# Performance work log

Measured on AMD Instinct MI355X. Metric: run time of the kernel, lower is better.

## Reference

```python
import jax, jax.numpy as jnp
import numpy as np

WL_W = 8  # weight bit-width (wl_weight)
WL_A = 8  # activation bit-width (wl_activate)


def _wage_q(x, bits):
    """WAGE quantizer with straight-through estimator.

    Rounds to a grid of step 1/2^(bits-1) and clips to (-1+delta, 1-delta),
    matching NeuroSim's wage_quantizer Q/C composition and the detach-based
    STE used in QConv2d/QLinear's training (inference=0) path.
    """
    s = 2.0 ** (bits - 1)
    delta = 1.0 / s
    q = jnp.clip(jnp.round(x * s) / s, -1.0 + delta, 1.0 - delta)
    return x + jax.lax.stop_gradient(q - x)


def _qconv(x, w):
    # quantize weights -> 3x3 conv (stride 1, pad 1) -> quantize activations
    wq = _wage_q(w, WL_W)
    y = jax.lax.conv_general_dilated(
        x, wq, window_strides=(1, 1), padding=((1, 1), (1, 1)),
        dimension_numbers=('NCHW', 'OIHW', 'NCHW'))
    return _wage_q(y, WL_A)


def setup_inputs() -> dict:
    key = jax.random.key(0)
    ks = jax.random.split(key, 9)
    x = jax.random.normal(ks[0], (16, 4, 256, 256), dtype=jnp.float32)
    w1 = jax.random.normal(ks[1], (32, 4, 3, 3), dtype=jnp.float32) * 0.2
    ws = {f"w{i}": jax.random.normal(ks[i], (32, 32, 3, 3), dtype=jnp.float32) * 0.1
          for i in range(2, 8)}
    wfc = jax.random.normal(ks[8], (1, 32), dtype=jnp.float32) * 0.2
    return {"x": x, "w1": w1, **ws, "wfc": wfc}


def reference(x, w1, w2, w3, w4, w5, w6, w7, wfc):
    # 7 stacked quantized 3x3 convs, channels 4->32->...->32
    for w in (w1, w2, w3, w4, w5, w6, w7):
        x = _qconv(x, w)                    # [B,32,256,256]
    x = jnp.max(x, axis=(2, 3))             # MaxPool2d(256,256) == global max -> [B,32]
    wq = _wage_q(wfc, WL_W)
    y = x @ wq.T                             # QLinear 32 -> 1, [B,1]
    return _wage_q(y, WL_A)
```

## Files before the change

### kernel.cpp

```cpp
#include <hip/hip_runtime.h>

#define BB 16
#define HH 256
#define WW 256
#define PC 258
#define PP ((size_t)(PC * PC))

typedef int i32x4 __attribute__((ext_vector_type(4)));
typedef int i32x16 __attribute__((ext_vector_type(16)));
typedef float f32x16 __attribute__((ext_vector_type(16)));
typedef _Float16 f16x8 __attribute__((ext_vector_type(8)));

__global__ __launch_bounds__(256) void prep_kernel(
    const float* __restrict__ x, const float* __restrict__ w1,
    const float* __restrict__ w2, const float* __restrict__ w3,
    const float* __restrict__ w4, const float* __restrict__ w5,
    const float* __restrict__ w6, const float* __restrict__ w7,
    const float* __restrict__ wfc,
    _Float16* __restrict__ pre, _Float16* __restrict__ frag1,
    signed char* __restrict__ wfr, int* __restrict__ wfcq,
    int* __restrict__ gmax, signed char* __restrict__ A0) {
  int bid = blockIdx.x, tid = threadIdx.x;
  if (bid < 4096) {
    int px = bid * 256 + tid;
    int b = px >> 16, rem = px & 65535;
    int y = rem >> 8, xc = rem & 255;
    const float* xp = x + (size_t)b * 4 * 65536 + rem;
    f16x8 o;
#pragma unroll
    for (int ic = 0; ic < 4; ++ic) {
      float v = xp[ic * 65536];
      _Float16 hf = (_Float16)v;
      float r = v - (float)hf;
      o[ic * 2] = hf;
      o[ic * 2 + 1] = (_Float16)r;
    }
    *(f16x8*)(pre + ((size_t)b * PP + (size_t)(y + 1) * PC + (xc + 1)) * 8) = o;
  } else if (bid < 4312) {
    int i = (bid - 4096) * 256 + tid;
    int layer = i / 9216, within = i - layer * 9216;
    const float* w = layer == 0 ? w2 : layer == 1 ? w3 : layer == 2 ? w4
                   : layer == 3 ? w5 : layer == 4 ? w6 : w7;
    int t = within >> 10;
    int l = (within >> 4) & 63;
    int j = within & 15;
    int ic = (l >> 5) * 16 + j;
    int oc = l & 31;
    int q = (int)rintf(w[oc * 288 + ic * 9 + t] * 128.0f);
    q = min(127, max(-127, q));
    wfr[(size_t)layer * 9216 + within] = (signed char)q;
  } else if (bid == 4312) {
    for (int p = tid; p < 384; p += 256) {
      int s = p >> 6, l = p & 63;
      int dr = s >> 1, pp = s & 1;
      int oc = l & 31, half = l >> 5;
      int dx = pp * 2 + half;
#pragma unroll
      for (int j = 0; j < 8; ++j) {
        int ic = j >> 1;
        _Float16 v = (_Float16)0.f;
        if (!(pp == 1 && half == 1)) {
          int q = (int)rintf(w1[oc * 36 + ic * 9 + dr * 3 + dx] * 128.0f);
          q = min(127, max(-127, q));
          v = (_Float16)((float)q * 0.0078125f);
        }
        frag1[s * 512 + l * 8 + j] = v;
      }
    }
    if (tid < 32) {
      int q = (int)rintf(wfc[tid] * 128.0f);
      q = min(127, max(-127, q));
      wfcq[tid] = q;
    }
    for (int i2 = tid; i2 < 512; i2 += 256) gmax[i2] = -128;
  } else {
    int idx = (bid - 4313) * 256 + tid;
    if (idx < 16448) {
      int img = idx / 1028, p = idx - img * 1028;
      int row, col;
      if (p < 258) { row = 0; col = p; }
      else if (p < 516) { row = 257; col = p - 258; }
      else { int q2 = p - 516; row = 1 + (q2 & 255); col = (q2 >> 8) ? 257 : 0; }
      size_t off = (size_t)img * PP + (size_t)row * PC + col;
      f16x8 z16 = {};
      *(f16x8*)(pre + off * 8) = z16;
      i32x4 z = {};
      ((i32x4*)(A0 + off * 32))[0] = z;
      ((i32x4*)(A0 + off * 32 + 16))[0] = z;
    }
  }
}

__global__ __launch_bounds__(256) void pad_kernel(signed char* __restrict__ A1) {
  int idx = blockIdx.x * 256 + threadIdx.x;
  if (idx < 16448) {
    int img = idx / 1028, p = idx - img * 1028;
    int row, col;
    if (p < 258) { row = 0; col = p; }
    else if (p < 516) { row = 257; col = p - 258; }
    else { int q2 = p - 516; row = 1 + (q2 & 255); col = (q2 >> 8) ? 257 : 0; }
    size_t off = (size_t)img * PP + (size_t)row * PC + col;
    i32x4 z = {};
    ((i32x4*)(A1 + off * 32))[0] = z;
    ((i32x4*)(A1 + off * 32 + 16))[0] = z;
  }
}

__device__ __forceinline__ int pack4(int q0, int q1, int q2, int q3) {
  return (q0 & 255) | ((q1 & 255) << 8) | ((q2 & 255) << 16) | ((q3 & 255) << 24);
}

__device__ __forceinline__ int quant1(int a) {
  int q = (a + 63 + ((a >> 7) & 1)) >> 7;
  return min(127, max(-127, q));
}

__device__ __forceinline__ int quant_max(const i32x16& acc, int mymax) {
#pragma unroll
  for (int r = 0; r < 16; ++r) mymax = max(mymax, quant1(acc[r]));
  return mymax;
}

__device__ __forceinline__ i32x4 half_swap(int v0, int v1, int v2, int v3, int hi) {
  int s0 = hi ? v0 : v2;
  int s1 = hi ? v1 : v3;
  int r0 = __shfl_xor(s0, 32);
  int r1 = __shfl_xor(s1, 32);
  i32x4 ch;
  ch.x = hi ? r0 : v0;
  ch.y = hi ? v2 : r0;
  ch.z = hi ? r1 : v1;
  ch.w = hi ? v3 : r1;
  return ch;
}

__global__ __launch_bounds__(256) void conv1_mfma_kernel(
    const _Float16* __restrict__ pre, const _Float16* __restrict__ frag1,
    signed char* __restrict__ out) {
  int tid = threadIdx.x;
  int wi = tid >> 6;
  int l = tid & 63;
  int lo = l & 31;
  int hi = l >> 5;
  int b = blockIdx.z;
  int h0 = blockIdx.y * 2;
  int wbase = blockIdx.x * 128 + wi * 32;
  int w = wbase + lo;

  const f16x8* fp = (const f16x8*)frag1;
  f16x8 bf[6];
#pragma unroll
  for (int s = 0; s < 6; ++s) bf[s] = fp[s * 64 + l];

  f32x16 acc0 = {}, acc1 = {};

#pragma unroll
  for (int r = 0; r < 4; ++r) {
    const _Float16* rp = pre + ((size_t)b * PP + (size_t)(h0 + r) * PC) * 8;
#pragma unroll
    for (int p = 0; p < 2; ++p) {
      int col = w + p * 2 + hi;
      f16x8 av = {};
      if (!(p == 1 && hi == 1))
        av = *(const f16x8*)(rp + (size_t)col * 8);
      if (r < 3) acc0 = __builtin_amdgcn_mfma_f32_32x32x16_f16(bf[r * 2 + p], av, acc0, 0, 0, 0);
      if (r > 0) acc1 = __builtin_amdgcn_mfma_f32_32x32x16_f16(bf[(r - 1) * 2 + p], av, acc1, 0, 0, 0);
    }
  }

#pragma unroll
  for (int rr = 0; rr < 2; ++rr) {
    const f32x16& acc = rr ? acc1 : acc0;
    int q[16];
#pragma unroll
    for (int r = 0; r < 16; ++r) {
      int t = (int)rintf(acc[r] * 128.0f);
      q[r] = min(127, max(-127, t));
    }
    int v0 = pack4(q[0], q[1], q[2], q[3]);
    int v1 = pack4(q[4], q[5], q[6], q[7]);
    int v2 = pack4(q[8], q[9], q[10], q[11]);
    int v3 = pack4(q[12], q[13], q[14], q[15]);
    i32x4 ch = half_swap(v0, v1, v2, v3, hi);
    *(i32x4*)(out + ((size_t)b * PP + (size_t)(h0 + rr + 1) * PC + (w + 1)) * 32 + hi * 16) = ch;
  }
}

template <int MODE>
__global__ __launch_bounds__(512, 4) void conv_fused_kernel(
    const signed char* __restrict__ in, const signed char* __restrict__ fragA,
    const signed char* __restrict__ fragB, signed char* __restrict__ out,
    int* __restrict__ gmax) {
  __shared__ int Lint[6 * 2 * PC * 4];
  __shared__ int red[8][32];

  int tid = threadIdx.x;
  int wi = tid >> 6;
  int l = tid & 63;
  int lo = l & 31;
  int hi = l >> 5;
  int b = blockIdx.y;
  int hs = blockIdx.x * 4;
  int w = wi * 32 + lo;

  if (tid < 24) {
    int rr = tid >> 2, half = (tid >> 1) & 1, cs = tid & 1;
    i32x4 z = {};
    *(i32x4*)&Lint[((rr * 2 + half) * PC + (cs ? 257 : 0)) * 4] = z;
  }

  const i32x4* fpA = (const i32x4*)fragA;
  i32x4 bw[9];
#pragma unroll
  for (int t = 0; t < 9; ++t) bw[t] = fpA[t * 64 + l];

  int lanep = (w << 5) + (hi << 4);

  auto rowptr = [&](int yy) -> const signed char* {
    int prow = min(max(yy + 1, 0), 257);
    return in + ((size_t)b * PP + (size_t)prow * PC) * 32 + lanep;
  };

  auto lds_store_row = [&](const i32x16& acc, int rrel, bool valid) {
    int v0 = pack4(quant1(acc[0]), quant1(acc[1]), quant1(acc[2]), quant1(acc[3]));
    int v1 = pack4(quant1(acc[4]), quant1(acc[5]), quant1(acc[6]), quant1(acc[7]));
    int v2 = pack4(quant1(acc[8]), quant1(acc[9]), quant1(acc[10]), quant1(acc[11]));
    int v3 = pack4(quant1(acc[12]), quant1(acc[13]), quant1(acc[14]), quant1(acc[15]));
    i32x4 ch = half_swap(v0, v1, v2, v3, hi);
    if (!valid) ch = i32x4{};
    *(i32x4*)&Lint[((rrel * 2 + hi) * PC + (w + 1)) * 4] = ch;
  };

#pragma unroll 1
  for (int p = 0; p < 3; ++p) {
    int ar0 = hs - 1 + 2 * p;
    const signed char* rp[4];
#pragma unroll
    for (int rr = 0; rr < 4; ++rr) rp[rr] = rowptr(ar0 - 1 + rr);
    i32x4 rin[4][3];
#pragma unroll
    for (int rr = 0; rr < 4; ++rr)
#pragma unroll
      for (int dx = 0; dx < 3; ++dx)
        rin[rr][dx] = *(const i32x4*)(rp[rr] + dx * 32);

    i32x16 acc0 = {}, acc1 = {};
#pragma unroll
    for (int t = 0; t < 9; ++t) {
      int dy = t / 3, dx = t % 3;
      acc0 = __builtin_amdgcn_mfma_i32_32x32x32_i8(bw[t], rin[dy][dx], acc0, 0, 0, 0);
      acc1 = __builtin_amdgcn_mfma_i32_32x32x32_i8(bw[t], rin[dy + 1][dx], acc1, 0, 0, 0);
    }
    lds_store_row(acc0, 2 * p, (unsigned)ar0 < 256u);
    lds_store_row(acc1, 2 * p + 1, (unsigned)(ar0 + 1) < 256u);
  }

  const i32x4* fpB = (const i32x4*)fragB;
#pragma unroll
  for (int t = 0; t < 9; ++t) bw[t] = fpB[t * 64 + l];
  __syncthreads();

  int mymax = -128;
#pragma unroll 1
  for (int p = 0; p < 2; ++p) {
    i32x4 tp[4][3];
#pragma unroll
    for (int rr = 0; rr < 4; ++rr) {
      int rrel = 2 * p + rr;
#pragma unroll
      for (int dx = 0; dx < 3; ++dx)
        tp[rr][dx] = *(const i32x4*)&Lint[((rrel * 2 + hi) * PC + (w + dx)) * 4];
    }
    i32x16 acc0 = {}, acc1 = {};
#pragma unroll
    for (int t = 0; t < 9; ++t) {
      int dy = t / 3, dx = t % 3;
      if (MODE == 1) {
        acc0 = __builtin_amdgcn_mfma_i32_32x32x32_i8(tp[dy][dx], bw[t], acc0, 0, 0, 0);
        acc1 = __builtin_amdgcn_mfma_i32_32x32x32_i8(tp[dy + 1][dx], bw[t], acc1, 0, 0, 0);
      } else {
        acc0 = __builtin_amdgcn_mfma_i32_32x32x32_i8(bw[t], tp[dy][dx], acc0, 0, 0, 0);
        acc1 = __builtin_amdgcn_mfma_i32_32x32x32_i8(bw[t], tp[dy + 1][dx], acc1, 0, 0, 0);
      }
    }
    if (MODE == 0) {
#pragma unroll
      for (int rr = 0; rr < 2; ++rr) {
        const i32x16& acc = rr ? acc1 : acc0;
        int v0 = pack4(quant1(acc[0]), quant1(acc[1]), quant1(acc[2]), quant1(acc[3]));
        int v1 = pack4(quant1(acc[4]), quant1(acc[5]), quant1(acc[6]), quant1(acc[7]));
        int v2 = pack4(quant1(acc[8]), quant1(acc[9]), quant1(acc[10]), quant1(acc[11]));
        int v3 = pack4(quant1(acc[12]), quant1(acc[13]), quant1(acc[14]), quant1(acc[15]));
        i32x4 ch = half_swap(v0, v1, v2, v3, hi);
        *(i32x4*)(out + ((size_t)b * PP + (size_t)(hs + 2 * p + rr + 1) * PC + (w + 1)) * 32 + hi * 16) = ch;
      }
    } else {
      mymax = quant_max(acc1, quant_max(acc0, mymax));
    }
  }

  if (MODE == 1) {
    mymax = max(mymax, __shfl_xor(mymax, 32));
    if (hi == 0) red[wi][lo] = mymax;
    __syncthreads();
    if (tid < 32) {
      int m = -128;
#pragma unroll
      for (int r = 0; r < 8; ++r) m = max(m, red[r][tid]);
      atomicMax(&gmax[b * 32 + tid], m);
    }
  }
}

__global__ void fc_kernel(const int* __restrict__ gmax, const int* __restrict__ wfcq,
                          float* __restrict__ out) {
  int b = threadIdx.x;
  if (b < BB) {
    int acc = 0;
#pragma unroll
    for (int c = 0; c < 32; ++c) acc += gmax[b * 32 + c] * wfcq[c];
    int q = (acc + 63 + ((acc >> 7) & 1)) >> 7;
    q = min(127, max(-127, q));
    out[b] = (float)q * 0.0078125f;
  }
}

extern "C" void kernel_launch(void* const* d_in, const int* in_sizes, int n_in,
                              void* d_out, int out_size, void* d_ws, size_t ws_size,
                              hipStream_t stream) {
  const float* x   = (const float*)d_in[0];
  const float* w1  = (const float*)d_in[1];
  const float* wfc = (const float*)d_in[8];

  char* ws = (char*)d_ws;
  const size_t ACTP = (size_t)BB * PP * 32;
  signed char* A0    = (signed char*)ws;
  signed char* A1    = (signed char*)(ws + ACTP);
  _Float16*    pre   = (_Float16*)A1;
  _Float16*    frag1 = (_Float16*)(ws + 2 * ACTP);
  signed char* wfr   = (signed char*)(ws + 2 * ACTP + 6144);
  int*         wfcq  = (int*)(ws + 2 * ACTP + 6144 + 6 * 9216);
  int*         gmax  = (int*)(ws + 2 * ACTP + 6144 + 6 * 9216 + 128);

  prep_kernel<<<4378, 256, 0, stream>>>(
      x, w1, (const float*)d_in[2], (const float*)d_in[3], (const float*)d_in[4],
      (const float*)d_in[5], (const float*)d_in[6], (const float*)d_in[7],
      wfc, pre, frag1, wfr, wfcq, gmax, A0);

  dim3 gridc1(2, 128, 16);
  conv1_mfma_kernel<<<gridc1, 256, 0, stream>>>(pre, frag1, A0);
  pad_kernel<<<65, 256, 0, stream>>>(A1);

  dim3 gf(64, 16);
  conv_fused_kernel<0><<<gf, 512, 0, stream>>>(A0, wfr + 0 * 9216, wfr + 1 * 9216, A1, nullptr);
  conv_fused_kernel<0><<<gf, 512, 0, stream>>>(A1, wfr + 2 * 9216, wfr + 3 * 9216, A0, nullptr);
  conv_fused_kernel<1><<<gf, 512, 0, stream>>>(A0, wfr + 4 * 9216, wfr + 5 * 9216, nullptr, gmax);
  fc_kernel<<<1, 64, 0, stream>>>(gmax, wfcq, (float*)d_out);
}
```

Baseline: 136.2 us.

## Double rows per block and stream the fused conv pair through an LDS ring

```diff
diff --git a/kernel.cpp b/kernel.cpp
--- a/kernel.cpp
+++ b/kernel.cpp
@@ -191,7 +191,7 @@
     const signed char* __restrict__ in, const signed char* __restrict__ fragA,
     const signed char* __restrict__ fragB, signed char* __restrict__ out,
     int* __restrict__ gmax) {
-  __shared__ int Lint[6 * 2 * PC * 4];
+  __shared__ int Aring[6 * 2 * PC * 4];
   __shared__ int red[8][32];
 
   int tid = threadIdx.x;
@@ -200,102 +200,104 @@
   int lo = l & 31;
   int hi = l >> 5;
   int b = blockIdx.y;
-  int hs = blockIdx.x * 4;
+  int hs = blockIdx.x * 8;
   int w = wi * 32 + lo;
 
   if (tid < 24) {
     int rr = tid >> 2, half = (tid >> 1) & 1, cs = tid & 1;
     i32x4 z = {};
-    *(i32x4*)&Lint[((rr * 2 + half) * PC + (cs ? 257 : 0)) * 4] = z;
+    *(i32x4*)&Aring[((rr * 2 + half) * PC + (cs ? 257 : 0)) * 4] = z;
   }
 
   const i32x4* fpA = (const i32x4*)fragA;
-  i32x4 bw[9];
-#pragma unroll
-  for (int t = 0; t < 9; ++t) bw[t] = fpA[t * 64 + l];
+  i32x4 bwA[9];
+#pragma unroll
+  for (int t = 0; t < 9; ++t) bwA[t] = fpA[t * 64 + l];
 
   int lanep = (w << 5) + (hi << 4);
 
-  auto rowptr = [&](int yy) -> const signed char* {
-    int prow = min(max(yy + 1, 0), 257);
+  auto rowptr = [&](int ar) -> const signed char* {
+    int prow = min(max(ar + 1, 0), 257);
     return in + ((size_t)b * PP + (size_t)prow * PC) * 32 + lanep;
   };
 
-  auto lds_store_row = [&](const i32x16& acc, int rrel, bool valid) {
+  auto ring_store = [&](const i32x16& acc, int slot, bool valid) {
     int v0 = pack4(quant1(acc[0]), quant1(acc[1]), quant1(acc[2]), quant1(acc[3]));
     int v1 = pack4(quant1(acc[4]), quant1(acc[5]), quant1(acc[6]), quant1(acc[7]));
     int v2 = pack4(quant1(acc[8]), quant1(acc[9]), quant1(acc[10]), quant1(acc[11]));
     int v3 = pack4(quant1(acc[12]), quant1(acc[13]), quant1(acc[14]), quant1(acc[15]));
     i32x4 ch = half_swap(v0, v1, v2, v3, hi);
     if (!valid) ch = i32x4{};
-    *(i32x4*)&Lint[((rrel * 2 + hi) * PC + (w + 1)) * 4] = ch;
+    *(i32x4*)&Aring[((slot * 2 + hi) * PC + (w + 1)) * 4] = ch;
   };
 
+  int mymax = -128;
+
 #pragma unroll 1
-  for (int p = 0; p < 3; ++p) {
-    int ar0 = hs - 1 + 2 * p;
-    const signed char* rp[4];
-#pragma unroll
-    for (int rr = 0; rr < 4; ++rr) rp[rr] = rowptr(ar0 - 1 + rr);
+  for (int k = 0; k < 5; ++k) {
+    int ar0 = hs - 1 + 2 * k;
     i32x4 rin[4][3];
 #pragma unroll
-    for (int rr = 0; rr < 4; ++rr)
-#pragma unroll
-      for (int dx = 0; dx < 3; ++dx)
-        rin[rr][dx] = *(const i32x4*)(rp[rr] + dx * 32);
-
+    for (int rr = 0; rr < 4; ++rr) {
+      const signed char* rp = rowptr(ar0 - 1 + rr);
+#pragma unroll
+      for (int dx = 0; dx < 3; ++dx) rin[rr][dx] = *(const i32x4*)(rp + dx * 32);
+    }
     i32x16 acc0 = {}, acc1 = {};
 #pragma unroll
     for (int t = 0; t < 9; ++t) {
       int dy = t / 3, dx = t % 3;
-      acc0 = __builtin_amdgcn_mfma_i32_32x32x32_i8(bw[t], rin[dy][dx], acc0, 0, 0, 0);
-      acc1 = __builtin_amdgcn_mfma_i32_32x32x32_i8(bw[t], rin[dy + 1][dx], acc1, 0, 0, 0);
-    }
-    lds_store_row(acc0, 2 * p, (unsigned)ar0 < 256u);
-    lds_store_row(acc1, 2 * p + 1, (unsigned)(ar0 + 1) < 256u);
-  }
-
-  const i32x4* fpB = (const i32x4*)fragB;
-#pragma unroll
-  for (int t = 0; t < 9; ++t) bw[t] = fpB[t * 64 + l];
-  __syncthreads();
-
-  int mymax = -128;
-#pragma unroll 1
-  for (int p = 0; p < 2; ++p) {
-    i32x4 tp[4][3];
-#pragma unroll
-    for (int rr = 0; rr < 4; ++rr) {
-      int rrel = 2 * p + rr;
-#pragma unroll
-      for (int dx = 0; dx < 3; ++dx)
-        tp[rr][dx] = *(const i32x4*)&Lint[((rrel * 2 + hi) * PC + (w + dx)) * 4];
-    }
-    i32x16 acc0 = {}, acc1 = {};
-#pragma unroll
-    for (int t = 0; t < 9; ++t) {
-      int dy = t / 3, dx = t % 3;
-      if (MODE == 1) {
-        acc0 = __builtin_amdgcn_mfma_i32_32x32x32_i8(tp[dy][dx], bw[t], acc0, 0, 0, 0);
-        acc1 = __builtin_amdgcn_mfma_i32_32x32x32_i8(tp[dy + 1][dx], bw[t], acc1, 0, 0, 0);
+      acc0 = __builtin_amdgcn_mfma_i32_32x32x32_i8(bwA[t], rin[dy][dx], acc0, 0, 0, 0);
+      acc1 = __builtin_amdgcn_mfma_i32_32x32x32_i8(bwA[t], rin[dy + 1][dx], acc1, 0, 0, 0);
+    }
+    ring_store(acc0, (2 * k) % 6, (unsigned)ar0 < 256u);
+    ring_store(acc1, (2 * k + 1) % 6, (unsigned)(ar0 + 1) < 256u);
+
+    __syncthreads();
+
+    if (k >= 1) {
+      int j = k - 1;
+      int pz = 0;
+      asm volatile("" : "+v"(pz));
+      const i32x4* fpB = (const i32x4*)fragB;
+      i32x4 bwB[9];
+#pragma unroll
+      for (int t = 0; t < 9; ++t) bwB[t] = fpB[t * 64 + l + pz];
+
+      i32x4 tp[4][3];
+#pragma unroll
+      for (int rr = 0; rr < 4; ++rr) {
+        int slot = (2 * j + rr) % 6;
+#pragma unroll
+        for (int dx = 0; dx < 3; ++dx)
+          tp[rr][dx] = *(const i32x4*)&Aring[((slot * 2 + hi) * PC + (w + dx)) * 4];
+      }
+      i32x16 c0 = {}, c1 = {};
+#pragma unroll
+      for (int t = 0; t < 9; ++t) {
+        int dy = t / 3, dx = t % 3;
+        if (MODE == 1) {
+          c0 = __builtin_amdgcn_mfma_i32_32x32x32_i8(tp[dy][dx], bwB[t], c0, 0, 0, 0);
+          c1 = __builtin_amdgcn_mfma_i32_32x32x32_i8(tp[dy + 1][dx], bwB[t], c1, 0, 0, 0);
+        } else {
+          c0 = __builtin_amdgcn_mfma_i32_32x32x32_i8(bwB[t], tp[dy][dx], c0, 0, 0, 0);
+          c1 = __builtin_amdgcn_mfma_i32_32x32x32_i8(bwB[t], tp[dy + 1][dx], c1, 0, 0, 0);
+        }
+      }
+      if (MODE == 0) {
+#pragma unroll
+        for (int rr = 0; rr < 2; ++rr) {
+          const i32x16& acc = rr ? c1 : c0;
+          int v0 = pack4(quant1(acc[0]), quant1(acc[1]), quant1(acc[2]), quant1(acc[3]));
+          int v1 = pack4(quant1(acc[4]), quant1(acc[5]), quant1(acc[6]), quant1(acc[7]));
+          int v2 = pack4(quant1(acc[8]), quant1(acc[9]), quant1(acc[10]), quant1(acc[11]));
+          int v3 = pack4(quant1(acc[12]), quant1(acc[13]), quant1(acc[14]), quant1(acc[15]));
+          i32x4 ch = half_swap(v0, v1, v2, v3, hi);
+          *(i32x4*)(out + ((size_t)b * PP + (size_t)(hs + 2 * j + rr + 1) * PC + (w + 1)) * 32 + hi * 16) = ch;
+        }
       } else {
-        acc0 = __builtin_amdgcn_mfma_i32_32x32x32_i8(bw[t], tp[dy][dx], acc0, 0, 0, 0);
-        acc1 = __builtin_amdgcn_mfma_i32_32x32x32_i8(bw[t], tp[dy + 1][dx], acc1, 0, 0, 0);
+        mymax = quant_max(c1, quant_max(c0, mymax));
       }
-    }
-    if (MODE == 0) {
-#pragma unroll
-      for (int rr = 0; rr < 2; ++rr) {
-        const i32x16& acc = rr ? acc1 : acc0;
-        int v0 = pack4(quant1(acc[0]), quant1(acc[1]), quant1(acc[2]), quant1(acc[3]));
-        int v1 = pack4(quant1(acc[4]), quant1(acc[5]), quant1(acc[6]), quant1(acc[7]));
-        int v2 = pack4(quant1(acc[8]), quant1(acc[9]), quant1(acc[10]), quant1(acc[11]));
-        int v3 = pack4(quant1(acc[12]), quant1(acc[13]), quant1(acc[14]), quant1(acc[15]));
-        i32x4 ch = half_swap(v0, v1, v2, v3, hi);
-        *(i32x4*)(out + ((size_t)b * PP + (size_t)(hs + 2 * p + rr + 1) * PC + (w + 1)) * 32 + hi * 16) = ch;
-      }
-    } else {
-      mymax = quant_max(acc1, quant_max(acc0, mymax));
     }
   }
 
@@ -351,7 +353,7 @@
   conv1_mfma_kernel<<<gridc1, 256, 0, stream>>>(pre, frag1, A0);
   pad_kernel<<<65, 256, 0, stream>>>(A1);
 
-  dim3 gf(64, 16);
+  dim3 gf(32, 16);
   conv_fused_kernel<0><<<gf, 512, 0, stream>>>(A0, wfr + 0 * 9216, wfr + 1 * 9216, A1, nullptr);
   conv_fused_kernel<0><<<gf, 512, 0, stream>>>(A1, wfr + 2 * 9216, wfr + 3 * 9216, A0, nullptr);
   conv_fused_kernel<1><<<gf, 512, 0, stream>>>(A0, wfr + 4 * 9216, wfr + 5 * 9216, nullptr, gmax);
```

New measurement: 132.9 us, median of 2. -2.4%, faster.
